# Optimization experiments

Hardware: AMD Instinct MI355X
Metric: run time of the kernel (lower is better)

The kernel has to match this reference:

```python
import jax, jax.numpy as jnp
import numpy as np

NUM_HEADS = 16
HEAD_DIM = 64
HIDDEN = NUM_HEADS * HEAD_DIM  # 1024


def get_rel_pos(q_size, k_size, rel_pos):
    # q_size == k_size here and rel_pos already has 2*size-1 rows, so the
    # F.interpolate(mode='linear') resize in the original is an identity.
    # relative_coords = q - k + (k_size - 1)  (scale factors are 1.0)
    coords = jnp.arange(q_size)[:, None] - jnp.arange(k_size)[None, :] + (k_size - 1)
    return rel_pos[coords]  # [q_size, k_size, head_dim]


def setup_inputs() -> dict:
    key = jax.random.key(0)
    ks = jax.random.split(key, 7)
    B, H, W = 4, 56, 28
    inp = {
        "hidden_states": jax.random.normal(ks[0], (B, H, W, HIDDEN), jnp.float32),
        "qkv_w": jax.random.normal(ks[1], (3 * HIDDEN, HIDDEN), jnp.float32) * 0.02,
        "qkv_b": jax.random.normal(ks[2], (3 * HIDDEN,), jnp.float32) * 0.02,
        "proj_w": jax.random.normal(ks[3], (HIDDEN, HIDDEN), jnp.float32) * 0.02,
        "proj_b": jax.random.normal(ks[4], (HIDDEN,), jnp.float32) * 0.02,
        "rel_pos_h": jax.random.normal(ks[5], (2 * H - 1, HEAD_DIM), jnp.float32) * 0.02,
        "rel_pos_w": jax.random.normal(ks[6], (2 * W - 1, HEAD_DIM), jnp.float32) * 0.02,
    }
    return inp


def reference(hidden_states, qkv_w, qkv_b, proj_w, proj_b, rel_pos_h, rel_pos_w):
    B, H, W, C = hidden_states.shape
    N = H * W
    scale = HEAD_DIM ** -0.5

    # qkv projection -> [3, B*heads, N, head_dim]
    qkv = hidden_states @ qkv_w.T + qkv_b
    qkv = qkv.reshape(B, N, 3, NUM_HEADS, HEAD_DIM).transpose(2, 0, 3, 1, 4)
    qkv = qkv.reshape(3, B * NUM_HEADS, N, HEAD_DIM)
    query, key_, value = qkv[0], qkv[1], qkv[2]

    # scaled dot-product scores, fully materialized as in the original
    attn = jnp.einsum('bqd,bkd->bqk', query * scale, key_)  # [B*heads, N, N]

    # decomposed relative position bias
    Rh = get_rel_pos(H, H, rel_pos_h)  # [H, H, d]
    Rw = get_rel_pos(W, W, rel_pos_w)  # [W, W, d]
    q_r = query.reshape(B * NUM_HEADS, H, W, HEAD_DIM)
    rel_h = jnp.einsum('bhwc,hkc->bhwk', q_r, Rh)  # [B*heads, H, W, H]
    rel_w = jnp.einsum('bhwc,wkc->bhwk', q_r, Rw)  # [B*heads, H, W, W]
    attn = attn.reshape(B * NUM_HEADS, H, W, H, W)
    attn = attn + rel_h[:, :, :, :, None] + rel_w[:, :, :, None, :]
    attn = attn.reshape(B * NUM_HEADS, N, N)

    attn = jax.nn.softmax(attn.astype(jnp.float32), axis=-1).astype(query.dtype)

    out = jnp.einsum('bqk,bkd->bqd', attn, value)
    out = out.reshape(B, NUM_HEADS, H, W, HEAD_DIM).transpose(0, 2, 3, 1, 4)
    out = out.reshape(B, H, W, C)
    out = out @ proj_w.T + proj_b
    return out
```

## Files before the change

### kernel.cpp

```cpp
#include <hip/hip_runtime.h>
#include <hip/hip_bf16.h>
#include <stdint.h>

typedef __bf16 bf16;
typedef __bf16 bf16x2 __attribute__((ext_vector_type(2)));
typedef __bf16 bf16x4 __attribute__((ext_vector_type(4)));
typedef __bf16 bf16x8 __attribute__((ext_vector_type(8)));
typedef float f32x4 __attribute__((ext_vector_type(4)));

#define AS1 __attribute__((address_space(1)))
#define AS3 __attribute__((address_space(3)))

static __device__ __forceinline__ void async_cp16(const bf16* g, bf16* l) {
    __builtin_amdgcn_global_load_lds((const AS1 void*)g, (AS3 void*)l, 16, 0, 0);
}

static __device__ __forceinline__ bf16x4 cvt4(f32x4 v) {
    bf16x4 r;
    r[0] = (bf16)v[0]; r[1] = (bf16)v[1]; r[2] = (bf16)v[2]; r[3] = (bf16)v[3];
    return r;
}

static __device__ __forceinline__ float fast_exp2(float x) {
#if __has_builtin(__builtin_amdgcn_exp2f)
    return __builtin_amdgcn_exp2f(x);
#else
    return __expf(x * 0.69314718056f);
#endif
}

__global__ __launch_bounds__(256) void cvt_all(
    const float* __restrict__ hs, const float* __restrict__ qw,
    const float* __restrict__ pw, bf16* __restrict__ dst) {
    const int H4 = 6272 * 1024 / 4, Q4 = 3072 * 1024 / 4, P4 = 1024 * 1024 / 4;
    const int total = H4 + Q4 + P4;
    int i = blockIdx.x * 256 + threadIdx.x;
    const int stride = gridDim.x * 256;
    for (; i < total; i += stride) {
        f32x4 v;
        if (i < H4)            v = ((const f32x4*)hs)[i];
        else if (i < H4 + Q4)  v = ((const f32x4*)qw)[i - H4];
        else                   v = ((const f32x4*)pw)[i - H4 - Q4];
        ((bf16x4*)dst)[i] = cvt4(v);
    }
}

__global__ __launch_bounds__(256) void setup_misc(
    bf16* __restrict__ Kone, bf16* __restrict__ slackA, bf16* __restrict__ slackB) {
    const int idx = blockIdx.x * 256 + threadIdx.x;
    if (idx < 6400) {
        const int key = idx >> 2, chunk = idx & 3;
        const int hk = key / 28;
        const int wk = key - hk * 28;
        const int kt = key >> 6;
        const int ha = (kt << 6) / 28;
        const int jw = 27 - wk;
        const int jh = 31 - (hk - ha);
        bf16x8 v;
#pragma unroll
        for (int e = 0; e < 8; e++) {
            const int j = chunk * 8 + e;
            v[e] = (j == jw || j == jh) ? (bf16)1.0f : (bf16)0.0f;
        }
        *(bf16x8*)&Kone[key * 32 + chunk * 8] = v;
    } else if (idx < 6656) {
        const int i = idx - 6400;
        bf16x8 z = {};
        *(bf16x8*)&slackA[i * 8] = z;
        *(bf16x8*)&slackB[i * 8] = z;
    }
}


#define QKV_EPILOGUE()                                                        \
    for (int nt = 0; nt < 4; nt++) {                                          \
        const int n_ = n0 + wn + nt * 16 + lm;                                \
        const float bv = bias[n_];                                            \
        const int s = n_ >> 10, rem = n_ & 1023;                              \
        const int h = rem >> 6, d = rem & 63;                                 \
        const float qsc = (s == 0) ? 0.18033688011112042f : 1.0f;             \
        for (int mt = 0; mt < 4; mt++) {                                      \
            for (int r = 0; r < 4; r++) {                                     \
                const int m_ = m0 + wm + mt * 16 + quad * 4 + r;              \
                const int b = m_ / 1568;                                      \
                const int pix = m_ - b * 1568;                                \
                const int g = b * 16 + h;                                     \
                const bf16 v = (bf16)((acc[mt][nt][r] + bv) * qsc);           \
                if (s == 0)      Qb[((size_t)g * 1568 + pix) * 64 + d] = v;   \
                else if (s == 1) Kb[((size_t)g * 1568 + pix) * 64 + d] = v;   \
                else {                                                        \
                    const int lk = pix & 31;                                  \
                    const int ppix = (pix & ~31) | ((lk & 15) << 1) | (lk >> 4); \
                    Vt[((size_t)g * 64 + d) * 1568 + ppix] = v;               \
                }                                                             \
            }                                                                 \
        }                                                                     \
    }


__global__ __launch_bounds__(256) void qkv_gemm_bf16(
    const bf16* __restrict__ A, const bf16* __restrict__ W,
    const float* __restrict__ bias, bf16* __restrict__ Qb,
    bf16* __restrict__ Kb, bf16* __restrict__ Vt) {
    __shared__ bf16 As[2][128 * 32];
    __shared__ bf16 Bs[2][128 * 32];
    const int t = threadIdx.x;
    const int wid = t >> 6, lane = t & 63;
    const int bid = blockIdx.x;
    const int widx = (bid & 7) * 147 + (bid >> 3);
    const int mt_ = widx / 24;
    const int m0 = mt_ * 128, n0 = (widx - mt_ * 24) * 128;
    const int wm = (wid & 1) * 64, wn = (wid >> 1) * 64;
    const int r_i = lane >> 2, c8 = (lane & 3) * 8;
    const int lm = lane & 15, quad = lane >> 4;

#define QKV_STAGE(buf, kk)                                                     \
    for (int i = 0; i < 2; i++) {                                              \
        const int blk = wid * 2 + i;                                           \
        async_cp16(A + (size_t)(m0 + blk * 16 + r_i) * 1024 + (kk) + c8,       \
                   &As[buf][blk * 512]);                                       \
        async_cp16(W + (size_t)(n0 + blk * 16 + r_i) * 1024 + (kk) + c8,       \
                   &Bs[buf][blk * 512]);                                       \
    }

    f32x4 acc[4][4] = {};
    QKV_STAGE(0, 0)
    __syncthreads();
    int cur = 0;
    for (int k0 = 0; k0 < 1024; k0 += 32) {
        if (k0 < 992) { QKV_STAGE(cur ^ 1, k0 + 32) }
        bf16x8 af[4], bfr[4];
        for (int x = 0; x < 4; x++) {
            af[x]  = *(const bf16x8*)&As[cur][(wm + x * 16 + lm) * 32 + quad * 8];
            bfr[x] = *(const bf16x8*)&Bs[cur][(wn + x * 16 + lm) * 32 + quad * 8];
        }
        for (int mt = 0; mt < 4; mt++)
            for (int nt = 0; nt < 4; nt++)
                acc[mt][nt] = __builtin_amdgcn_mfma_f32_16x16x32_bf16(af[mt], bfr[nt], acc[mt][nt], 0, 0, 0);
        __syncthreads();
        cur ^= 1;
    }
#undef QKV_STAGE
    QKV_EPILOGUE()
}

__global__ __launch_bounds__(256) void qkv_gemm_f32(
    const float* __restrict__ A, const float* __restrict__ W,
    const float* __restrict__ bias, bf16* __restrict__ Qb,
    bf16* __restrict__ Kb, bf16* __restrict__ Vt) {
    __shared__ bf16 As[2][128 * 32];
    __shared__ bf16 Bs[2][128 * 32];
    const int t = threadIdx.x;
    const int wid = t >> 6, lane = t & 63;
    const int bid = blockIdx.x;
    const int widx = (bid & 7) * 147 + (bid >> 3);
    const int mt_ = widx / 24;
    const int m0 = mt_ * 128, n0 = (widx - mt_ * 24) * 128;
    const int wm = (wid & 1) * 64, wn = (wid >> 1) * 64;
    const int lm = lane & 15, quad = lane >> 4;

#define QKVF_STAGE(buf, kk)                                                    \
    for (int i = 0; i < 4; i++) {                                              \
        const int idx = t + i * 256;                                           \
        const int row = idx >> 3, c4 = (idx & 7) * 4;                          \
        const f32x4 av = *(const f32x4*)&A[(size_t)(m0 + row) * 1024 + (kk) + c4]; \
        const f32x4 wv = *(const f32x4*)&W[(size_t)(n0 + row) * 1024 + (kk) + c4]; \
        *(bf16x4*)&As[buf][row * 32 + c4] = cvt4(av);                          \
        *(bf16x4*)&Bs[buf][row * 32 + c4] = cvt4(wv);                          \
    }

    f32x4 acc[4][4] = {};
    QKVF_STAGE(0, 0)
    __syncthreads();
    int cur = 0;
    for (int k0 = 0; k0 < 1024; k0 += 32) {
        if (k0 < 992) { QKVF_STAGE(cur ^ 1, k0 + 32) }
        bf16x8 af[4], bfr[4];
        for (int x = 0; x < 4; x++) {
            af[x]  = *(const bf16x8*)&As[cur][(wm + x * 16 + lm) * 32 + quad * 8];
            bfr[x] = *(const bf16x8*)&Bs[cur][(wn + x * 16 + lm) * 32 + quad * 8];
        }
        for (int mt = 0; mt < 4; mt++)
            for (int nt = 0; nt < 4; nt++)
                acc[mt][nt] = __builtin_amdgcn_mfma_f32_16x16x32_bf16(af[mt], bfr[nt], acc[mt][nt], 0, 0, 0);
        __syncthreads();
        cur ^= 1;
    }
#undef QKVF_STAGE
    QKV_EPILOGUE()
}

__global__ __launch_bounds__(256) void flash_attn(
    const bf16* __restrict__ Qb, const bf16* __restrict__ Kb,
    const bf16* __restrict__ Vt, const float* __restrict__ rph,
    const float* __restrict__ rpw, const bf16* __restrict__ Kone,
    bf16* __restrict__ AO) {
    const int x = blockIdx.x;
    const int xcd = x & 7, j = x >> 3;
    const int g = xcd * 8 + j / 25;
    const int qblk = j - (j / 25) * 25;
    const int q0 = qblk * 64;
    const int hqb = q0 / 28;

    __shared__ __align__(16) char smem[51200];
    bf16* Th = (bf16*)smem;
    const char* ThC = (const char*)smem;
    char* B = smem + 8192;
    bf16* Qs  = (bf16*)(B + 32768);
    bf16* RPh = (bf16*)(B + 0);
    bf16* RPw = (bf16*)(B + 9216);
    float* TwF = (float*)(B + 18432);
    bf16* TwS = (bf16*)(B + 33280);

    const int t = threadIdx.x, wid = t >> 6, lane = t & 63;
    const int lm = lane & 15, quad = lane >> 4;
    const int qbase_l = wid * 16 + quad * 4;
    const int swz = (lm & 7) << 4;
    const int l3 = lane >> 3, l7 = lane & 7;
    const int swe = ((l7 ^ l3) << 3);

    const bf16* kSrc[2];
    const bf16* vSrc[2];
#pragma unroll
    for (int i = 0; i < 2; i++) {
        kSrc[i] = Kb + ((size_t)g * 1568 + wid * 16 + i * 8 + l3) * 64 + swe;
        vSrc[i] = Vt + ((size_t)g * 64 + wid * 16 + i * 8 + l3) * 1568 + swe;
    }

    for (int c = t; c < 512; c += 256) {
        const int row = c >> 3, col = (c & 7) * 8;
        const int qg = min(q0 + row, 1567);
        *(bf16x8*)&Qs[row * 72 + col] =
            *(const bf16x8*)&Qb[((size_t)g * 1568 + qg) * 64 + col];
    }
    for (int c = t; c < 1024; c += 256) {
        const int row = c >> 4, col = (c & 15) * 4;
        const int rg = min(hqb + row, 110);
        *(bf16x4*)&RPh[row * 72 + col] = cvt4(*(const f32x4*)&rph[rg * 64 + col]);
    }
    __syncthreads();

    const int qrow_l = wid * 16 + lm;
    const bf16x8 qf0 = *(const bf16x8*)&Qs[qrow_l * 72 + quad * 8];
    const bf16x8 qf1 = *(const bf16x8*)&Qs[qrow_l * 72 + 32 + quad * 8];
    const int qgl = min(q0 + qrow_l, 1567);
    const int thb2 = (qrow_l * 64 + (qgl / 28 - hqb) + 54) * 2;

    for (int c = t; c < 1024; c += 256) {
        const int row = c >> 4, col = (c & 15) * 4;
        const int rg = min(row, 54);
        *(bf16x4*)&RPw[row * 72 + col] = cvt4(*(const f32x4*)&rpw[rg * 64 + col]);
    }
    f32x4 acch[4];
#pragma unroll
    for (int nt = 0; nt < 4; nt++) {
        const bf16x8 b0 = *(const bf16x8*)&RPh[(nt * 16 + lm) * 72 + quad * 8];
        const bf16x8 b1 = *(const bf16x8*)&RPh[(nt * 16 + lm) * 72 + 32 + quad * 8];
        f32x4 a = {};
        a = __builtin_amdgcn_mfma_f32_16x16x32_bf16(qf0, b0, a, 0, 0, 0);
        a = __builtin_amdgcn_mfma_f32_16x16x32_bf16(qf1, b1, a, 0, 0, 0);
        acch[nt] = a;
    }
    __syncthreads();

#pragma unroll
    for (int nt = 0; nt < 4; nt++) {
        const int c = nt * 16 + lm;
        if (c < 59) {
#pragma unroll
            for (int r = 0; r < 4; r++)
                Th[(qbase_l + r) * 64 + c + 2] = (bf16)(acch[nt][r] * 8.0f);
        }
    }
    if (lm == 0) {
#pragma unroll
        for (int r = 0; r < 4; r++) {
            Th[(qbase_l + r) * 64 + 0] = (bf16)0.0f;
            Th[(qbase_l + r) * 64 + 1] = (bf16)0.0f;
        }
    }
#pragma unroll
    for (int nt = 0; nt < 4; nt++) {
        const bf16x8 b0 = *(const bf16x8*)&RPw[(nt * 16 + lm) * 72 + quad * 8];
        const bf16x8 b1 = *(const bf16x8*)&RPw[(nt * 16 + lm) * 72 + 32 + quad * 8];
        f32x4 a = {};
        a = __builtin_amdgcn_mfma_f32_16x16x32_bf16(qf0, b0, a, 0, 0, 0);
        a = __builtin_amdgcn_mfma_f32_16x16x32_bf16(qf1, b1, a, 0, 0, 0);
        const int c = nt * 16 + lm;
        if (c < 55) {
#pragma unroll
            for (int r = 0; r < 4; r++)
                TwF[(qbase_l + r) * 58 + c] = a[r] * 8.0f;
        }
    }
    __syncthreads();

    {
        const int row = t >> 2, chunk = t & 3;
        const int qg = min(q0 + row, 1567);
        const int wq = qg % 28;
        const float* src = &TwF[row * 58 + wq];
        bf16x8 v;
        if (chunk < 3) {
#pragma unroll
            for (int e = 0; e < 8; e++) v[e] = (bf16)src[chunk * 8 + e];
        } else {
#pragma unroll
            for (int e = 0; e < 4; e++) v[e] = (bf16)src[24 + e];
#pragma unroll
            for (int e = 4; e < 8; e++) v[e] = (bf16)0.0f;
        }
        *(bf16x8*)&TwS[row * 32 + chunk * 8] = v;
    }
    __syncthreads();

    const bf16x8 qt_mine = *(const bf16x8*)&TwS[qrow_l * 32 + quad * 8];

#pragma unroll
    for (int i = 0; i < 2; i++) {
        async_cp16(kSrc[i], (bf16*)(B + (wid * 2 + i) * 1024));
        async_cp16(vSrc[i], (bf16*)(B + 16384 + (wid * 2 + i) * 1024));
        kSrc[i] += 4096;
        vSrc[i] += 64;
    }
    const bf16* kop = Kone + lm * 32 + quad * 8;
    bf16x8 ko[4];
#pragma unroll
    for (int f = 0; f < 4; f++) ko[f] = *(const bf16x8*)(kop + f * 512);
    __syncthreads();

    f32x4 o[4] = {};
    f32x4 lsum = {};
    const f32x4 zero4 = {};
    bf16x8 ones;
#pragma unroll
    for (int i = 0; i < 8; i++) ones[i] = (bf16)1.0f;

    bf16* P0w = (bf16*)(B + 32768) + wid * 640;
    bf16* P1w = (bf16*)(B + 37888) + wid * 640;

    int curo = 0;
    for (int kt = 0; kt < 25; kt++) {
        bf16x8 qf2 = qt_mine;
        if (quad == 3) {
            const int ha = (kt << 6) / 28;
            const char* tp = ThC + (thb2 - (ha << 1));
            qf2[4] = *(const bf16*)(tp);
            qf2[5] = *(const bf16*)(tp + 2);
            qf2[6] = *(const bf16*)(tp + 4);
            qf2[7] = *(const bf16*)(tp + 6);
        }

        if (kt < 24) {
            const int nxto = curo ^ 8192;
#pragma unroll
            for (int i = 0; i < 2; i++) {
                async_cp16(kSrc[i], (bf16*)(B + nxto + (wid * 2 + i) * 1024));
                async_cp16(vSrc[i], (bf16*)(B + 16384 + nxto + (wid * 2 + i) * 1024));
                kSrc[i] += 4096;
                vSrc[i] += 64;
            }
        }

        __builtin_amdgcn_s_setprio(1);
        f32x4 s[4];
#pragma unroll
        for (int f = 0; f < 4; f++)
            s[f] = __builtin_amdgcn_mfma_f32_16x16x32_bf16(qf2, ko[f], zero4, 0, 0, 0);
        {
            const char* KsB = B + curo;
            const int x0 = (quad * 16) ^ swz;
#pragma unroll
            for (int f = 0; f < 4; f++) {
                const char* rp = KsB + (f * 16 + lm) * 128;
                const bf16x8 ka = *(const bf16x8*)(rp + x0);
                const bf16x8 kb2 = *(const bf16x8*)(rp + (x0 ^ 64));
                s[f] = __builtin_amdgcn_mfma_f32_16x16x32_bf16(qf0, ka, s[f], 0, 0, 0);
                s[f] = __builtin_amdgcn_mfma_f32_16x16x32_bf16(qf1, kb2, s[f], 0, 0, 0);
            }
        }
        __builtin_amdgcn_s_setprio(0);

        if (kt < 24) {
            kop += 2048;
#pragma unroll
            for (int f = 0; f < 4; f++) ko[f] = *(const bf16x8*)(kop + f * 512);
        }

        if (kt == 24) {
#pragma unroll
            for (int r = 0; r < 4; r++) { s[2][r] = -30000.0f; s[3][r] = -30000.0f; }
        }

#pragma unroll
        for (int r = 0; r < 4; r++) {
            const float a0 = fast_exp2(s[0][r]);
            const float a1 = fast_exp2(s[1][r]);
            bf16x2 pp; pp[0] = (bf16)a0; pp[1] = (bf16)a1;
            *(bf16x2*)&P0w[(quad * 4 + r) * 40 + lm * 2] = pp;
            const float b0 = fast_exp2(s[2][r]);
            const float b1 = fast_exp2(s[3][r]);
            bf16x2 qq; qq[0] = (bf16)b0; qq[1] = (bf16)b1;
            *(bf16x2*)&P1w[(quad * 4 + r) * 40 + lm * 2] = qq;
        }
        __asm__ volatile("s_waitcnt lgkmcnt(0)" ::: "memory");
        const bf16x8 pf0 = *(const bf16x8*)&P0w[lm * 40 + quad * 8];
        const bf16x8 pf1 = *(const bf16x8*)&P1w[lm * 40 + quad * 8];
        lsum = __builtin_amdgcn_mfma_f32_16x16x32_bf16(pf0, ones, lsum, 0, 0, 0);
        lsum = __builtin_amdgcn_mfma_f32_16x16x32_bf16(pf1, ones, lsum, 0, 0, 0);
        __builtin_amdgcn_s_setprio(1);
        {
            const char* VsB = B + 16384 + curo;
#pragma unroll
            for (int dt = 0; dt < 4; dt++) {
                const bf16x8 vf = *(const bf16x8*)(VsB + (dt * 16 + lm) * 128 +
                                                   ((quad * 16) ^ swz));
                o[dt] = __builtin_amdgcn_mfma_f32_16x16x32_bf16(pf0, vf, o[dt], 0, 0, 0);
            }
#pragma unroll
            for (int dt = 0; dt < 4; dt++) {
                const bf16x8 vf = *(const bf16x8*)(VsB + (dt * 16 + lm) * 128 +
                                                   ((64 + quad * 16) ^ swz));
                o[dt] = __builtin_amdgcn_mfma_f32_16x16x32_bf16(pf1, vf, o[dt], 0, 0, 0);
            }
        }
        __builtin_amdgcn_s_setprio(0);

        if (kt < 24) {
            __syncthreads();
            curo ^= 8192;
        }
    }

    if (q0 + wid * 16 < 1568) {
        const int bo = g >> 4, hh = g & 15;
#pragma unroll
        for (int r = 0; r < 4; r++) {
            const float inv = 1.0f / lsum[r];
            const size_t base = ((size_t)bo * 1568 + q0 + qbase_l + r) * 1024 + hh * 64;
#pragma unroll
            for (int dt = 0; dt < 4; dt++)
                AO[base + dt * 16 + lm] = (bf16)(o[dt][r] * inv);
        }
    }
}

__global__ __launch_bounds__(256) void proj_gemm_bf16(
    const bf16* __restrict__ A, const bf16* __restrict__ W,
    const float* __restrict__ bias, float* __restrict__ out) {
    __shared__ bf16 As[2][128 * 32];
    __shared__ bf16 Bs[2][128 * 32];
    const int t = threadIdx.x;
    const int wid = t >> 6, lane = t & 63;
    const int bid = blockIdx.x;
    const int widx = (bid & 7) * 49 + (bid >> 3);
    const int m0 = (widx >> 3) * 128, n0 = (widx & 7) * 128;
    const int wm = (wid & 1) * 64, wn = (wid >> 1) * 64;
    const int r_i = lane >> 2, c8 = (lane & 3) * 8;
    const int lm = lane & 15, quad = lane >> 4;

#define PROJ_STAGE(buf, kk)                                                    \
    for (int i = 0; i < 2; i++) {                                              \
        const int blk = wid * 2 + i;                                           \
        async_cp16(A + (size_t)(m0 + blk * 16 + r_i) * 1024 + (kk) + c8,       \
                   &As[buf][blk * 512]);                                       \
        async_cp16(W + (size_t)(n0 + blk * 16 + r_i) * 1024 + (kk) + c8,       \
                   &Bs[buf][blk * 512]);                                       \
    }

    f32x4 acc[4][4] = {};
    PROJ_STAGE(0, 0)
    __syncthreads();
    int cur = 0;
    for (int k0 = 0; k0 < 1024; k0 += 32) {
        if (k0 < 992) { PROJ_STAGE(cur ^ 1, k0 + 32) }
        bf16x8 af[4], bfr[4];
        for (int x = 0; x < 4; x++) {
            af[x]  = *(const bf16x8*)&As[cur][(wm + x * 16 + lm) * 32 + quad * 8];
            bfr[x] = *(const bf16x8*)&Bs[cur][(wn + x * 16 + lm) * 32 + quad * 8];
        }
        for (int mt = 0; mt < 4; mt++)
            for (int nt = 0; nt < 4; nt++)
                acc[mt][nt] = __builtin_amdgcn_mfma_f32_16x16x32_bf16(af[mt], bfr[nt], acc[mt][nt], 0, 0, 0);
        __syncthreads();
        cur ^= 1;
    }
#undef PROJ_STAGE
    for (int nt = 0; nt < 4; nt++) {
        const int n_ = n0 + wn + nt * 16 + lm;
        const float bv = bias[n_];
        for (int mt = 0; mt < 4; mt++)
            for (int r = 0; r < 4; r++) {
                const int m_ = m0 + wm + mt * 16 + quad * 4 + r;
                out[(size_t)m_ * 1024 + n_] = acc[mt][nt][r] + bv;
            }
    }
}

__global__ __launch_bounds__(256) void proj_gemm_f32(
    const bf16* __restrict__ A, const float* __restrict__ W,
    const float* __restrict__ bias, float* __restrict__ out) {
    __shared__ bf16 As[2][128 * 32];
    __shared__ bf16 Bs[2][128 * 32];
    const int t = threadIdx.x;
    const int wid = t >> 6, lane = t & 63;
    const int bid = blockIdx.x;
    const int widx = (bid & 7) * 49 + (bid >> 3);
    const int m0 = (widx >> 3) * 128, n0 = (widx & 7) * 128;
    const int wm = (wid & 1) * 64, wn = (wid >> 1) * 64;
    const int r_i = lane >> 2, c8 = (lane & 3) * 8;
    const int lm = lane & 15, quad = lane >> 4;

#define PROJF_STAGE(buf, kk)                                                   \
    for (int i = 0; i < 2; i++) {                                              \
        const int blk = wid * 2 + i;                                           \
        async_cp16(A + (size_t)(m0 + blk * 16 + r_i) * 1024 + (kk) + c8,       \
                   &As[buf][blk * 512]);                                       \
    }                                                                          \
    for (int i = 0; i < 4; i++) {                                              \
        const int idx = t + i * 256;                                           \
        const int row = idx >> 3, c4 = (idx & 7) * 4;                          \
        const f32x4 wv = *(const f32x4*)&W[(size_t)(n0 + row) * 1024 + (kk) + c4]; \
        *(bf16x4*)&Bs[buf][row * 32 + c4] = cvt4(wv);                          \
    }

    f32x4 acc[4][4] = {};
    PROJF_STAGE(0, 0)
    __syncthreads();
    int cur = 0;
    for (int k0 = 0; k0 < 1024; k0 += 32) {
        if (k0 < 992) { PROJF_STAGE(cur ^ 1, k0 + 32) }
        bf16x8 af[4], bfr[4];
        for (int x = 0; x < 4; x++) {
            af[x]  = *(const bf16x8*)&As[cur][(wm + x * 16 + lm) * 32 + quad * 8];
            bfr[x] = *(const bf16x8*)&Bs[cur][(wn + x * 16 + lm) * 32 + quad * 8];
        }
        for (int mt = 0; mt < 4; mt++)
            for (int nt = 0; nt < 4; nt++)
                acc[mt][nt] = __builtin_amdgcn_mfma_f32_16x16x32_bf16(af[mt], bfr[nt], acc[mt][nt], 0, 0, 0);
        __syncthreads();
        cur ^= 1;
    }
#undef PROJF_STAGE
    for (int nt = 0; nt < 4; nt++) {
        const int n_ = n0 + wn + nt * 16 + lm;
        const float bv = bias[n_];
        for (int mt = 0; mt < 4; mt++)
            for (int r = 0; r < 4; r++) {
                const int m_ = m0 + wm + mt * 16 + quad * 4 + r;
                out[(size_t)m_ * 1024 + n_] = acc[mt][nt][r] + bv;
            }
    }
}

extern "C" void kernel_launch(void* const* d_in, const int* in_sizes, int n_in,
                              void* d_out, int out_size, void* d_ws, size_t ws_size,
                              hipStream_t stream) {
    const float* hs     = (const float*)d_in[0];
    const float* qkv_w  = (const float*)d_in[1];
    const float* qkv_b  = (const float*)d_in[2];
    const float* proj_w = (const float*)d_in[3];
    const float* proj_b = (const float*)d_in[4];
    const float* rph    = (const float*)d_in[5];
    const float* rpw    = (const float*)d_in[6];
    float* out = (float*)d_out;

    const size_t GQ  = (size_t)64 * 1568 * 64;
    const size_t SL  = 2048;
    const size_t N_KONE = (size_t)1600 * 32;
    const size_t N_HS = (size_t)6272 * 1024;
    const size_t N_QW = (size_t)3072 * 1024;
    const size_t N_PW = (size_t)1024 * 1024;
    bf16* Qb = (bf16*)d_ws;
    bf16* Kb = Qb + GQ;
    bf16* Vt = Kb + GQ + SL;
    bf16* AO = Vt + GQ + SL;
    bf16* Kone = AO + GQ;
    bf16* hs_bf    = Kone + N_KONE;
    bf16* qkvw_bf  = hs_bf + N_HS;
    bf16* projw_bf = qkvw_bf + N_QW;
    const size_t need = (4 * GQ + 2 * SL + N_KONE + N_HS + N_QW + N_PW) * sizeof(bf16);

    if (ws_size >= need) {
        setup_misc<<<26, 256, 0, stream>>>(Kone, Kb + GQ, Vt + GQ);
        cvt_all<<<1024, 256, 0, stream>>>(hs, qkv_w, proj_w, hs_bf);
        qkv_gemm_bf16<<<1176, 256, 0, stream>>>(hs_bf, qkvw_bf, qkv_b, Qb, Kb, Vt);
        flash_attn<<<1600, 256, 0, stream>>>(Qb, Kb, Vt, rph, rpw, Kone, AO);
        proj_gemm_bf16<<<392, 256, 0, stream>>>(AO, projw_bf, proj_b, out);
    } else {
        setup_misc<<<26, 256, 0, stream>>>(Kone, Kb + GQ, Vt + GQ);
        qkv_gemm_f32<<<1176, 256, 0, stream>>>(hs, qkv_w, qkv_b, Qb, Kb, Vt);
        flash_attn<<<1600, 256, 0, stream>>>(Qb, Kb, Vt, rph, rpw, Kone, AO);
        proj_gemm_f32<<<392, 256, 0, stream>>>(AO, proj_w, proj_b, out);
    }
}
```

Baseline: 294.9 us.

## Triple-buffer LDS staging with partial vmcnt waits in bf16 QKV and proj GEMMs

Moves the bf16 QKV and projection GEMMs from double to triple LDS buffering, keeping two async global-to-LDS stages in flight. Full __syncthreads are replaced by explicit s_waitcnt vmcnt(4) plus s_barrier, so only the oldest stage must land before compute. The aim is to hide global load latency behind MFMA work. It costs 50% more LDS per block, which may cut occupancy, and correctness rests on the hand-counted vmcnt values.

```diff
diff --git a/kernel.cpp b/kernel.cpp
--- a/kernel.cpp
+++ b/kernel.cpp
@@ -102,8 +102,8 @@
     const bf16* __restrict__ A, const bf16* __restrict__ W,
     const float* __restrict__ bias, bf16* __restrict__ Qb,
     bf16* __restrict__ Kb, bf16* __restrict__ Vt) {
-    __shared__ bf16 As[2][128 * 32];
-    __shared__ bf16 Bs[2][128 * 32];
+    __shared__ bf16 As[3][128 * 32];
+    __shared__ bf16 Bs[3][128 * 32];
     const int t = threadIdx.x;
     const int wid = t >> 6, lane = t & 63;
     const int bid = blockIdx.x;
@@ -125,10 +125,15 @@
 
     f32x4 acc[4][4] = {};
     QKV_STAGE(0, 0)
-    __syncthreads();
+    QKV_STAGE(1, 32)
+    __asm__ volatile("s_waitcnt vmcnt(4)" ::: "memory");
+    __builtin_amdgcn_s_barrier();
     int cur = 0;
-    for (int k0 = 0; k0 < 1024; k0 += 32) {
-        if (k0 < 992) { QKV_STAGE(cur ^ 1, k0 + 32) }
+    for (int t32 = 0; t32 < 32; t32++) {
+        if (t32 < 30) {
+            const int nxt = (cur >= 1) ? cur - 1 : 2;
+            QKV_STAGE(nxt, t32 * 32 + 64)
+        }
         bf16x8 af[4], bfr[4];
         for (int x = 0; x < 4; x++) {
             af[x]  = *(const bf16x8*)&As[cur][(wm + x * 16 + lm) * 32 + quad * 8];
@@ -137,8 +142,12 @@
         for (int mt = 0; mt < 4; mt++)
             for (int nt = 0; nt < 4; nt++)
                 acc[mt][nt] = __builtin_amdgcn_mfma_f32_16x16x32_bf16(af[mt], bfr[nt], acc[mt][nt], 0, 0, 0);
-        __syncthreads();
-        cur ^= 1;
+        if (t32 < 31) {
+            if (t32 < 30) { __asm__ volatile("s_waitcnt vmcnt(4)" ::: "memory"); }
+            else          { __asm__ volatile("s_waitcnt vmcnt(0)" ::: "memory"); }
+            __builtin_amdgcn_s_barrier();
+        }
+        cur = (cur < 2) ? cur + 1 : 0;
     }
 #undef QKV_STAGE
     QKV_EPILOGUE()
@@ -448,8 +457,8 @@
 __global__ __launch_bounds__(256) void proj_gemm_bf16(
     const bf16* __restrict__ A, const bf16* __restrict__ W,
     const float* __restrict__ bias, float* __restrict__ out) {
-    __shared__ bf16 As[2][128 * 32];
-    __shared__ bf16 Bs[2][128 * 32];
+    __shared__ bf16 As[3][128 * 32];
+    __shared__ bf16 Bs[3][128 * 32];
     const int t = threadIdx.x;
     const int wid = t >> 6, lane = t & 63;
     const int bid = blockIdx.x;
@@ -470,10 +479,15 @@
 
     f32x4 acc[4][4] = {};
     PROJ_STAGE(0, 0)
-    __syncthreads();
+    PROJ_STAGE(1, 32)
+    __asm__ volatile("s_waitcnt vmcnt(4)" ::: "memory");
+    __builtin_amdgcn_s_barrier();
     int cur = 0;
-    for (int k0 = 0; k0 < 1024; k0 += 32) {
-        if (k0 < 992) { PROJ_STAGE(cur ^ 1, k0 + 32) }
+    for (int t32 = 0; t32 < 32; t32++) {
+        if (t32 < 30) {
+            const int nxt = (cur >= 1) ? cur - 1 : 2;
+            PROJ_STAGE(nxt, t32 * 32 + 64)
+        }
         bf16x8 af[4], bfr[4];
         for (int x = 0; x < 4; x++) {
             af[x]  = *(const bf16x8*)&As[cur][(wm + x * 16 + lm) * 32 + quad * 8];
@@ -482,8 +496,12 @@
         for (int mt = 0; mt < 4; mt++)
             for (int nt = 0; nt < 4; nt++)
                 acc[mt][nt] = __builtin_amdgcn_mfma_f32_16x16x32_bf16(af[mt], bfr[nt], acc[mt][nt], 0, 0, 0);
-        __syncthreads();
-        cur ^= 1;
+        if (t32 < 31) {
+            if (t32 < 30) { __asm__ volatile("s_waitcnt vmcnt(4)" ::: "memory"); }
+            else          { __asm__ volatile("s_waitcnt vmcnt(0)" ::: "memory"); }
+            __builtin_amdgcn_s_barrier();
+        }
+        cur = (cur < 2) ? cur + 1 : 0;
     }
 #undef PROJ_STAGE
     for (int nt = 0; nt < 4; nt++) {
```

Result: slower. 304.2 us (+3.2%).
